# Kernel optimization log

Hardware: AMD Instinct MI355X
Metric: run time of the kernel (lower is better)

The kernel has to match this reference:

```python
import jax, jax.numpy as jnp
import numpy as np

P, K, T, C, F = 2048, 8, 32, 16384, 128  # paths, channels/path, steps/channel, channels, feature


def setup_inputs() -> dict:
    key = jax.random.key(0)
    k0, k1, k2, k3, k4, k5, k6 = jax.random.split(key, 7)
    s = 1.0 / np.sqrt(F)  # PyTorch GRU init scale
    return {
        "path_h0": jax.random.normal(k0, (P, F), dtype=jnp.float32),
        "channel_features": jax.random.normal(k1, (C, T, F), dtype=jnp.float32) * 0.1,
        "w_ih": jax.random.uniform(k2, (3 * F, F), minval=-s, maxval=s, dtype=jnp.float32),
        "w_hh": jax.random.uniform(k3, (3 * F, F), minval=-s, maxval=s, dtype=jnp.float32),
        "b_ih": jax.random.uniform(k4, (3 * F,), minval=-s, maxval=s, dtype=jnp.float32),
        "b_hh": jax.random.uniform(k5, (3 * F,), minval=-s, maxval=s, dtype=jnp.float32),
        "channel_idx": jax.random.randint(k6, (P, K), 0, C, dtype=jnp.int64),
    }


def reference(path_h0, channel_features, w_ih, w_hh, b_ih, b_hh, channel_idx):
    # Gather each path's K neighbor-channel sequences and concatenate in time:
    # the original code threads the path hidden state through the GRU over each
    # channel sequence in order, which equals one GRU pass over the concatenation.
    seq = channel_features[channel_idx]            # [P, K, T, F]
    p, f = path_h0.shape
    seq = seq.reshape(p, -1, f)                    # [P, K*T, F]
    # Precompute input-gate projections for all timesteps at once.
    x_gates = jnp.einsum("ptf,gf->ptg", seq, w_ih) + b_ih  # [P, K*T, 3F]

    def step(h, xg):
        hg = h @ w_hh.T + b_hh                     # [P, 3F]
        xr, xz, xn = jnp.split(xg, 3, axis=-1)
        hr, hz, hn = jnp.split(hg, 3, axis=-1)
        r = jax.nn.sigmoid(xr + hr)
        z = jax.nn.sigmoid(xz + hz)
        n = jnp.tanh(xn + r * hn)
        h_new = (1.0 - z) * n + z * h              # PyTorch GRU update
        return h_new, None

    h_final, _ = jax.lax.scan(step, path_h0, jnp.swapaxes(x_gates, 0, 1))
    return h_final                                  # [P, F] updated path states
```

## Files before the change

### kernel.cpp

```cpp
#include <hip/hip_runtime.h>
#include <cstdint>
#include <cstddef>

#define PP 2048
#define KK 8
#define TT 32
#define FF 128
#define MB 8
#define NBLK (PP/MB)
#define NTHR 512
#define NSTEP (KK*TT)

typedef __attribute__((ext_vector_type(8))) short short8;
typedef __attribute__((ext_vector_type(4))) float f32x4;

__device__ __forceinline__ uint32_t fbits(float x){ union{float f;uint32_t u;}c;c.f=x;return c.u; }
__device__ __forceinline__ uint32_t rne16(uint32_t u){
    return (u + 0x7fffu + ((u >> 16) & 1u)) >> 16;
}
__device__ __forceinline__ short bf_rne(float x){ return (short)rne16(fbits(x)); }
__device__ __forceinline__ uint32_t pk_rne(float a, float b){
    return rne16(fbits(a)) | (rne16(fbits(b)) << 16);
}
__device__ __forceinline__ float sigm(float x){
    float t = __expf(-x);
    return __builtin_amdgcn_rcpf(1.f + t);
}
__device__ __forceinline__ float tanh_fast(float x){
    float e = __expf(-2.f * x);
    return __builtin_amdgcn_rcpf(1.f + e) * 2.f - 1.f;
}

__global__ __launch_bounds__(NTHR, 2) void gru_mfma4(
    const float* __restrict__ h0,
    const float* __restrict__ feat,
    const float* __restrict__ w_ih,
    const float* __restrict__ w_hh,
    const float* __restrict__ b_ih,
    const float* __restrict__ b_hh,
    const int* __restrict__ idx,
    float* __restrict__ out)
{
    const int tid  = threadIdx.x;
    const int w    = tid >> 6;
    const int lane = tid & 63;
    const int q    = lane >> 4;
    const int nl   = lane & 15;
    const int p0   = blockIdx.x * MB;

    __shared__ __align__(16) short xfr[2][4][32][8];
    __shared__ __align__(16) short hhi[2][4][32][8];
    __shared__ int cix[MB][KK];

    short8 wbi[3][4], wbh[3][4];
#pragma unroll
    for (int tt = 0; tt < 3; ++tt) {
        const int g = (w + 8 * tt) * 16 + nl;
#pragma unroll
        for (int c = 0; c < 4; ++c) {
            const float* wi = w_ih + (size_t)g * FF + c * 32 + q * 8;
            const float* wh = w_hh + (size_t)g * FF + c * 32 + q * 8;
            short8 a, b;
#pragma unroll
            for (int j = 0; j < 8; ++j) { a[j] = bf_rne(wi[j]); b[j] = bf_rne(wh[j]); }
            wbi[tt][c] = a; wbh[tt][c] = b;
        }
    }
    const int fcol = w * 16 + nl;
    const float bR  = b_ih[fcol] + b_hh[fcol];
    const float bZ  = b_ih[FF + fcol] + b_hh[FF + fcol];
    const float bNi = b_ih[2 * FF + fcol];
    const float bNh = b_hh[2 * FF + fcol];

    if (tid < MB * KK) cix[tid >> 3][tid & 7] = idx[(p0 + (tid >> 3)) * KK + (tid & 7)];
    __syncthreads();

    const int qqF = 2 * (w & 1) + (nl >> 3);
    const int jF  = nl & 7;
    const int cF  = w >> 1;
    const int pb  = 4 * (q & 1) + 2 * (q >> 1);
    int sp[2];
#pragma unroll
    for (int j = 0; j < 2; ++j) {
        const int p = pb + j;
        sp[j] = (p >> 2) + 2 * ((p & 3) ^ qqF) + 8 * qqF;
    }

    const int row = lane & 15;
    const int pr  = (row < 8) ? row : ((row & 4) | ((row & 3) ^ 2));
    const int xslot = pr + 8 * q;
    const int hslot = (pr >> 2) + 2 * ((pr & 3) ^ q) + 8 * q;

    float hm[2];
#pragma unroll
    for (int j = 0; j < 2; ++j) {
        const float h = h0[(size_t)(p0 + pb + j) * FF + fcol];
        hm[j] = h;
        hhi[0][cF][sp[j]][jF] = bf_rne(h);
    }

    const bool stg    = tid < 256;
    const int  c_s    = tid >> 6;
    const int  r6     = tid & 63;
    const int  slot_s = r6 >> 1;
    const int  half   = r6 & 1;
    const int  path_s = slot_s & 7;
    const int  qq_s   = slot_s >> 3;
    const int  k0s    = c_s * 32 + qq_s * 8 + 4 * half;

    float4 xp;
    if (stg) {
        const int ch = cix[path_s][0];
        const float4 v = *(const float4*)(feat + (size_t)ch * (TT * FF) + k0s);
        uint2 pkd = { pk_rne(v.x, v.y), pk_rne(v.z, v.w) };
        *(uint2*)&xfr[0][c_s][slot_s][4 * half] = pkd;
        xp = *(const float4*)(feat + (size_t)ch * (TT * FF) + FF + k0s);
    }
    __syncthreads();

    int curb = 0;
    for (int s = 0; s < NSTEP; ++s) {
        const int nxtb = curb ^ 1;

        if (stg) {
            if (s < NSTEP - 1) {
                uint2 pkd = { pk_rne(xp.x, xp.y), pk_rne(xp.z, xp.w) };
                *(uint2*)&xfr[nxtb][c_s][slot_s][4 * half] = pkd;
            }
            if (s < NSTEP - 2) {
                const int u = s + 2;
                const int ch = cix[path_s][u >> 5];
                xp = *(const float4*)(feat + (size_t)ch * (TT * FF) + (u & 31) * FF + k0s);
            }
        }

        short8 xa[4], ha[4];
#pragma unroll
        for (int c = 0; c < 4; ++c) {
            xa[c] = *(const short8*)&xfr[curb][c][xslot][0];
            ha[c] = *(const short8*)&hhi[curb][c][hslot][0];
        }

        f32x4 gR, gZ, axN, ahN;
        {
            f32x4 a0 = {0.f,0.f,0.f,0.f}, a1 = {0.f,0.f,0.f,0.f};
            a0 = __builtin_amdgcn_mfma_f32_16x16x32_bf16(xa[0], wbi[0][0], a0, 0, 0, 0);
            a0 = __builtin_amdgcn_mfma_f32_16x16x32_bf16(xa[1], wbi[0][1], a0, 0, 0, 0);
            a1 = __builtin_amdgcn_mfma_f32_16x16x32_bf16(xa[2], wbi[0][2], a1, 0, 0, 0);
            a1 = __builtin_amdgcn_mfma_f32_16x16x32_bf16(xa[3], wbi[0][3], a1, 0, 0, 0);
            a0 = __builtin_amdgcn_mfma_f32_16x16x32_bf16(ha[0], wbh[0][0], a0, 0, 0, 0);
            a0 = __builtin_amdgcn_mfma_f32_16x16x32_bf16(ha[1], wbh[0][1], a0, 0, 0, 0);
            a1 = __builtin_amdgcn_mfma_f32_16x16x32_bf16(ha[2], wbh[0][2], a1, 0, 0, 0);
            a1 = __builtin_amdgcn_mfma_f32_16x16x32_bf16(ha[3], wbh[0][3], a1, 0, 0, 0);
            gR = a0 + a1;
        }
        {
            f32x4 a0 = {0.f,0.f,0.f,0.f}, a1 = {0.f,0.f,0.f,0.f};
            a0 = __builtin_amdgcn_mfma_f32_16x16x32_bf16(xa[0], wbi[1][0], a0, 0, 0, 0);
            a0 = __builtin_amdgcn_mfma_f32_16x16x32_bf16(xa[1], wbi[1][1], a0, 0, 0, 0);
            a1 = __builtin_amdgcn_mfma_f32_16x16x32_bf16(xa[2], wbi[1][2], a1, 0, 0, 0);
            a1 = __builtin_amdgcn_mfma_f32_16x16x32_bf16(xa[3], wbi[1][3], a1, 0, 0, 0);
            a0 = __builtin_amdgcn_mfma_f32_16x16x32_bf16(ha[0], wbh[1][0], a0, 0, 0, 0);
            a0 = __builtin_amdgcn_mfma_f32_16x16x32_bf16(ha[1], wbh[1][1], a0, 0, 0, 0);
            a1 = __builtin_amdgcn_mfma_f32_16x16x32_bf16(ha[2], wbh[1][2], a1, 0, 0, 0);
            a1 = __builtin_amdgcn_mfma_f32_16x16x32_bf16(ha[3], wbh[1][3], a1, 0, 0, 0);
            gZ = a0 + a1;
        }
        {
            f32x4 a0 = {0.f,0.f,0.f,0.f}, a1 = {0.f,0.f,0.f,0.f};
            f32x4 u0 = {0.f,0.f,0.f,0.f}, u1 = {0.f,0.f,0.f,0.f};
            a0 = __builtin_amdgcn_mfma_f32_16x16x32_bf16(xa[0], wbi[2][0], a0, 0, 0, 0);
            a0 = __builtin_amdgcn_mfma_f32_16x16x32_bf16(xa[1], wbi[2][1], a0, 0, 0, 0);
            a1 = __builtin_amdgcn_mfma_f32_16x16x32_bf16(xa[2], wbi[2][2], a1, 0, 0, 0);
            a1 = __builtin_amdgcn_mfma_f32_16x16x32_bf16(xa[3], wbi[2][3], a1, 0, 0, 0);
            u0 = __builtin_amdgcn_mfma_f32_16x16x32_bf16(ha[0], wbh[2][0], u0, 0, 0, 0);
            u0 = __builtin_amdgcn_mfma_f32_16x16x32_bf16(ha[1], wbh[2][1], u0, 0, 0, 0);
            u1 = __builtin_amdgcn_mfma_f32_16x16x32_bf16(ha[2], wbh[2][2], u1, 0, 0, 0);
            u1 = __builtin_amdgcn_mfma_f32_16x16x32_bf16(ha[3], wbh[2][3], u1, 0, 0, 0);
            axN = a0 + a1; ahN = u0 + u1;
        }

#pragma unroll
        for (int j = 0; j < 2; ++j) {
            const float rg  = sigm(gR[j] + bR);
            const float zg  = sigm(gZ[j] + bZ);
            const float np_ = axN[j] + bNi + rg * (ahN[j] + bNh);
            const float ng  = tanh_fast(np_);
            const float h   = ng + zg * (hm[j] - ng);
            hm[j] = h;
            hhi[nxtb][cF][sp[j]][jF] = bf_rne(h);
        }
        __syncthreads();
        curb = nxtb;
    }

#pragma unroll
    for (int j = 0; j < 2; ++j)
        out[(size_t)(p0 + pb + j) * FF + fcol] = hm[j];
}

extern "C" void kernel_launch(void* const* d_in, const int* in_sizes, int n_in,
                              void* d_out, int out_size, void* d_ws, size_t ws_size,
                              hipStream_t stream) {
    const float* h0   = (const float*)d_in[0];
    const float* feat = (const float*)d_in[1];
    const float* wih  = (const float*)d_in[2];
    const float* whh  = (const float*)d_in[3];
    const float* bih  = (const float*)d_in[4];
    const float* bhh  = (const float*)d_in[5];
    const int*   idx  = (const int*)d_in[6];
    float*       out  = (float*)d_out;

    gru_mfma4<<<dim3(NBLK), dim3(NTHR), 0, stream>>>(
        h0, feat, wih, whh, bih, bhh, idx, out);
}
```

Baseline: 486.0 us.

## Precompute next step's input-gate MFMAs off the recurrent critical path

Result: no change. 480.0 us (-1.2%).

```diff
diff --git a/kernel.cpp b/kernel.cpp
--- a/kernel.cpp
+++ b/kernel.cpp
@@ -31,7 +31,7 @@
     return __builtin_amdgcn_rcpf(1.f + e) * 2.f - 1.f;
 }
 
-__global__ __launch_bounds__(NTHR, 2) void gru_mfma4(
+__global__ __launch_bounds__(NTHR, 2) void gru_mfma5(
     const float* __restrict__ h0,
     const float* __restrict__ feat,
     const float* __restrict__ w_ih,
@@ -73,7 +73,6 @@
     const float bNh = b_hh[2 * FF + fcol];
 
     if (tid < MB * KK) cix[tid >> 3][tid & 7] = idx[(p0 + (tid >> 3)) * KK + (tid & 7)];
-    __syncthreads();
 
     const int qqF = 2 * (w & 1) + (nl >> 3);
     const int jF  = nl & 7;
@@ -108,88 +107,94 @@
     const int  qq_s   = slot_s >> 3;
     const int  k0s    = c_s * 32 + qq_s * 8 + 4 * half;
 
+    __syncthreads();
+
     float4 xp;
     if (stg) {
         const int ch = cix[path_s][0];
-        const float4 v = *(const float4*)(feat + (size_t)ch * (TT * FF) + k0s);
-        uint2 pkd = { pk_rne(v.x, v.y), pk_rne(v.z, v.w) };
-        *(uint2*)&xfr[0][c_s][slot_s][4 * half] = pkd;
-        xp = *(const float4*)(feat + (size_t)ch * (TT * FF) + FF + k0s);
+        const float* base = feat + (size_t)ch * (TT * FF) + k0s;
+        const float4 v0 = *(const float4*)(base);
+        const float4 v1 = *(const float4*)(base + FF);
+        uint2 p0d = { pk_rne(v0.x, v0.y), pk_rne(v0.z, v0.w) };
+        uint2 p1d = { pk_rne(v1.x, v1.y), pk_rne(v1.z, v1.w) };
+        *(uint2*)&xfr[0][c_s][slot_s][4 * half] = p0d;
+        *(uint2*)&xfr[1][c_s][slot_s][4 * half] = p1d;
+        xp = *(const float4*)(base + 2 * FF);
     }
     __syncthreads();
+
+    f32x4 paxR, paxZ, paxN;
+    {
+        short8 xa0[4];
+#pragma unroll
+        for (int c = 0; c < 4; ++c) xa0[c] = *(const short8*)&xfr[0][c][xslot][0];
+        __syncthreads();
+
+        f32x4 r = {bR, bR, bR, bR}, z = {bZ, bZ, bZ, bZ}, n = {bNi, bNi, bNi, bNi};
+#pragma unroll
+        for (int c = 0; c < 4; ++c) {
+            r = __builtin_amdgcn_mfma_f32_16x16x32_bf16(xa0[c], wbi[0][c], r, 0, 0, 0);
+            z = __builtin_amdgcn_mfma_f32_16x16x32_bf16(xa0[c], wbi[1][c], z, 0, 0, 0);
+            n = __builtin_amdgcn_mfma_f32_16x16x32_bf16(xa0[c], wbi[2][c], n, 0, 0, 0);
+        }
+        paxR = r; paxZ = z; paxN = n;
+    }
 
     int curb = 0;
     for (int s = 0; s < NSTEP; ++s) {
         const int nxtb = curb ^ 1;
 
         if (stg) {
-            if (s < NSTEP - 1) {
+            if (s < NSTEP - 2) {
                 uint2 pkd = { pk_rne(xp.x, xp.y), pk_rne(xp.z, xp.w) };
-                *(uint2*)&xfr[nxtb][c_s][slot_s][4 * half] = pkd;
+                *(uint2*)&xfr[curb][c_s][slot_s][4 * half] = pkd;
             }
-            if (s < NSTEP - 2) {
-                const int u = s + 2;
+            if (s < NSTEP - 3) {
+                const int u = s + 3;
                 const int ch = cix[path_s][u >> 5];
                 xp = *(const float4*)(feat + (size_t)ch * (TT * FF) + (u & 31) * FF + k0s);
             }
         }
 
-        short8 xa[4], ha[4];
+        short8 ha[4];
+#pragma unroll
+        for (int c = 0; c < 4; ++c) ha[c] = *(const short8*)&hhi[curb][c][hslot][0];
+        short8 xn[4];
+        if (s < NSTEP - 1) {
+#pragma unroll
+            for (int c = 0; c < 4; ++c) xn[c] = *(const short8*)&xfr[nxtb][c][xslot][0];
+        }
+
+        f32x4 ahN = {bNh, bNh, bNh, bNh};
 #pragma unroll
         for (int c = 0; c < 4; ++c) {
-            xa[c] = *(const short8*)&xfr[curb][c][xslot][0];
-            ha[c] = *(const short8*)&hhi[curb][c][hslot][0];
-        }
-
-        f32x4 gR, gZ, axN, ahN;
-        {
-            f32x4 a0 = {0.f,0.f,0.f,0.f}, a1 = {0.f,0.f,0.f,0.f};
-            a0 = __builtin_amdgcn_mfma_f32_16x16x32_bf16(xa[0], wbi[0][0], a0, 0, 0, 0);
-            a0 = __builtin_amdgcn_mfma_f32_16x16x32_bf16(xa[1], wbi[0][1], a0, 0, 0, 0);
-            a1 = __builtin_amdgcn_mfma_f32_16x16x32_bf16(xa[2], wbi[0][2], a1, 0, 0, 0);
-            a1 = __builtin_amdgcn_mfma_f32_16x16x32_bf16(xa[3], wbi[0][3], a1, 0, 0, 0);
-            a0 = __builtin_amdgcn_mfma_f32_16x16x32_bf16(ha[0], wbh[0][0], a0, 0, 0, 0);
-            a0 = __builtin_amdgcn_mfma_f32_16x16x32_bf16(ha[1], wbh[0][1], a0, 0, 0, 0);
-            a1 = __builtin_amdgcn_mfma_f32_16x16x32_bf16(ha[2], wbh[0][2], a1, 0, 0, 0);
-            a1 = __builtin_amdgcn_mfma_f32_16x16x32_bf16(ha[3], wbh[0][3], a1, 0, 0, 0);
-            gR = a0 + a1;
-        }
-        {
-            f32x4 a0 = {0.f,0.f,0.f,0.f}, a1 = {0.f,0.f,0.f,0.f};
-            a0 = __builtin_amdgcn_mfma_f32_16x16x32_bf16(xa[0], wbi[1][0], a0, 0, 0, 0);
-            a0 = __builtin_amdgcn_mfma_f32_16x16x32_bf16(xa[1], wbi[1][1], a0, 0, 0, 0);
-            a1 = __builtin_amdgcn_mfma_f32_16x16x32_bf16(xa[2], wbi[1][2], a1, 0, 0, 0);
-            a1 = __builtin_amdgcn_mfma_f32_16x16x32_bf16(xa[3], wbi[1][3], a1, 0, 0, 0);
-            a0 = __builtin_amdgcn_mfma_f32_16x16x32_bf16(ha[0], wbh[1][0], a0, 0, 0, 0);
-            a0 = __builtin_amdgcn_mfma_f32_16x16x32_bf16(ha[1], wbh[1][1], a0, 0, 0, 0);
-            a1 = __builtin_amdgcn_mfma_f32_16x16x32_bf16(ha[2], wbh[1][2], a1, 0, 0, 0);
-            a1 = __builtin_amdgcn_mfma_f32_16x16x32_bf16(ha[3], wbh[1][3], a1, 0, 0, 0);
-            gZ = a0 + a1;
-        }
-        {
-            f32x4 a0 = {0.f,0.f,0.f,0.f}, a1 = {0.f,0.f,0.f,0.f};
-            f32x4 u0 = {0.f,0.f,0.f,0.f}, u1 = {0.f,0.f,0.f,0.f};
-            a0 = __builtin_amdgcn_mfma_f32_16x16x32_bf16(xa[0], wbi[2][0], a0, 0, 0, 0);
-            a0 = __builtin_amdgcn_mfma_f32_16x16x32_bf16(xa[1], wbi[2][1], a0, 0, 0, 0);
-            a1 = __builtin_amdgcn_mfma_f32_16x16x32_bf16(xa[2], wbi[2][2], a1, 0, 0, 0);
-            a1 = __builtin_amdgcn_mfma_f32_16x16x32_bf16(xa[3], wbi[2][3], a1, 0, 0, 0);
-            u0 = __builtin_amdgcn_mfma_f32_16x16x32_bf16(ha[0], wbh[2][0], u0, 0, 0, 0);
-            u0 = __builtin_amdgcn_mfma_f32_16x16x32_bf16(ha[1], wbh[2][1], u0, 0, 0, 0);
-            u1 = __builtin_amdgcn_mfma_f32_16x16x32_bf16(ha[2], wbh[2][2], u1, 0, 0, 0);
-            u1 = __builtin_amdgcn_mfma_f32_16x16x32_bf16(ha[3], wbh[2][3], u1, 0, 0, 0);
-            axN = a0 + a1; ahN = u0 + u1;
+            paxR = __builtin_amdgcn_mfma_f32_16x16x32_bf16(ha[c], wbh[0][c], paxR, 0, 0, 0);
+            paxZ = __builtin_amdgcn_mfma_f32_16x16x32_bf16(ha[c], wbh[1][c], paxZ, 0, 0, 0);
+            ahN  = __builtin_amdgcn_mfma_f32_16x16x32_bf16(ha[c], wbh[2][c], ahN, 0, 0, 0);
         }
 
 #pragma unroll
         for (int j = 0; j < 2; ++j) {
-            const float rg  = sigm(gR[j] + bR);
-            const float zg  = sigm(gZ[j] + bZ);
-            const float np_ = axN[j] + bNi + rg * (ahN[j] + bNh);
+            const float rg  = sigm(paxR[j]);
+            const float zg  = sigm(paxZ[j]);
+            const float np_ = paxN[j] + rg * ahN[j];
             const float ng  = tanh_fast(np_);
             const float h   = ng + zg * (hm[j] - ng);
             hm[j] = h;
             hhi[nxtb][cF][sp[j]][jF] = bf_rne(h);
         }
+
+        if (s < NSTEP - 1) {
+            f32x4 r = {bR, bR, bR, bR}, z = {bZ, bZ, bZ, bZ}, n = {bNi, bNi, bNi, bNi};
+#pragma unroll
+            for (int c = 0; c < 4; ++c) {
+                r = __builtin_amdgcn_mfma_f32_16x16x32_bf16(xn[c], wbi[0][c], r, 0, 0, 0);
+                z = __builtin_amdgcn_mfma_f32_16x16x32_bf16(xn[c], wbi[1][c], z, 0, 0, 0);
+                n = __builtin_amdgcn_mfma_f32_16x16x32_bf16(xn[c], wbi[2][c], n, 0, 0, 0);
+            }
+            paxR = r; paxZ = z; paxN = n;
+        }
+
         __syncthreads();
         curb = nxtb;
     }
@@ -211,6 +216,6 @@
     const int*   idx  = (const int*)d_in[6];
     float*       out  = (float*)d_out;
 
-    gru_mfma4<<<dim3(NBLK), dim3(NTHR), 0, stream>>>(
+    gru_mfma5<<<dim3(NBLK), dim3(NTHR), 0, stream>>>(
         h0, feat, wih, whh, bih, bhh, idx, out);
 }
```
